# Kernel optimization log

Measured on AMD Instinct MI355X. Metric: run time of the kernel, lower is better.

The kernel has to match this reference:

```python
import jax, jax.numpy as jnp
import numpy as np

D = 1024

def setup_inputs() -> dict:
    key = jax.random.key(0)
    ks = jax.random.split(key, 12)
    B, N, d = 4, 4096, D
    init_std = 0.02 / np.sqrt(d)  # matches _init_weights for value_proj / o_proj
    inp = {
        "h": jax.random.normal(ks[0], (B, N, d), dtype=jnp.float32),
        # relation_encoder: Linear(d, d//2) -> GELU -> Linear(d//2, 1)  (weights stored [in, out])
        "W_re1": jax.random.normal(ks[1], (d, d // 2), dtype=jnp.float32) * 0.02,
        "b_re1": jnp.zeros((d // 2,), dtype=jnp.float32),
        "W_re2": jax.random.normal(ks[2], (d // 2, 1), dtype=jnp.float32) * 0.02,
        "b_re2": jnp.zeros((1,), dtype=jnp.float32),
        # value_proj: Linear(d, d, bias=False), init std = 0.02/sqrt(d)
        "W_v": jax.random.normal(ks[3], (d, d), dtype=jnp.float32) * init_std,
        # relation_transform: Linear(2d, d) -> GELU -> Linear(d, d)
        "W_rt1": jax.random.normal(ks[4], (2 * d, d), dtype=jnp.float32) * 0.02,
        "b_rt1": jnp.zeros((d,), dtype=jnp.float32),
        "W_rt2": jax.random.normal(ks[5], (d, d), dtype=jnp.float32) * 0.02,
        "b_rt2": jnp.zeros((d,), dtype=jnp.float32),
        # o_proj: Linear(d, d, bias=False), init std = 0.02/sqrt(d)
        "W_o": jax.random.normal(ks[6], (d, d), dtype=jnp.float32) * init_std,
    }
    return inp


def reference(h, W_re1, b_re1, W_re2, b_re2, W_v, W_rt1, b_rt1, W_rt2, b_rt2, W_o):
    B, N, d = h.shape
    # relation_encoder MLP -> scalar logit per token (torch GELU is exact erf form)
    hidden = jax.nn.gelu(jnp.einsum('bnd,dk->bnk', h, W_re1) + b_re1, approximate=False)
    relation_logits = (jnp.einsum('bnk,ko->bno', hidden, W_re2) + b_re2)[..., 0]  # [B, N]
    relation_strength = jax.nn.sigmoid(relation_logits)  # [B, N]
    # pointer targets: round(sigmoid * (N-1)) clamped (jnp.round == torch.round, half-to-even)
    relation_targets = jnp.clip(
        jnp.round(relation_strength * (N - 1)).astype(jnp.int32), 0, N - 1
    )  # [B, N]
    # per-token gather of target hidden state within each batch row
    target_features = jnp.take_along_axis(h, relation_targets[..., None], axis=1)  # [B, N, d]
    source_values = jnp.einsum('bnd,de->bne', h, W_v)
    target_values = jnp.einsum('bnd,de->bne', target_features, W_v)
    relation_input = jnp.concatenate([source_values, target_values], axis=-1)  # [B, N, 2d]
    relation_output = jax.nn.gelu(
        jnp.einsum('bnf,fe->bne', relation_input, W_rt1) + b_rt1, approximate=False
    )
    relation_output = jnp.einsum('bne,ef->bnf', relation_output, W_rt2) + b_rt2
    z = jnp.einsum('bnd,de->bne', relation_output, W_o)  # [B, N, d]
    return (z, relation_targets, relation_strength)
```

## Files before the change

kernel.cpp:

```cpp
#include <hip/hip_runtime.h>
#include <math.h>
#include <type_traits>

#define DMODEL 1024
#define NSEQ   4096
#define MTOT   16384

typedef unsigned short ushortT;
typedef __attribute__((ext_vector_type(8))) short short8;
typedef __attribute__((ext_vector_type(4))) float f32x4;

__device__ __forceinline__ float gelu_f(float x) {
    return 0.5f * x * (1.0f + erff(x * 0.70710678118654752440f));
}
__device__ __forceinline__ double gelu_d(double x) {
    return 0.5 * x * (1.0 + erf(x * 0.70710678118654752440));
}
__device__ __forceinline__ ushortT f2bf(float f) {
    unsigned u = __float_as_uint(f);
    u += 0x7FFFu + ((u >> 16) & 1u);
    return (ushortT)(u >> 16);
}
__device__ __forceinline__ float bf2f(ushortT b) {
    return __uint_as_float(((unsigned)b) << 16);
}
__device__ __forceinline__ void gload16(const void* g, void* l) {
    __builtin_amdgcn_global_load_lds(
        (const __attribute__((address_space(1))) unsigned*)g,
        (__attribute__((address_space(3))) unsigned*)l, 16, 0, 0);
}

enum { EPI_BF16 = 0, EPI_GELU_BIAS_BF16 = 1, EPI_BIAS_F32 = 2, EPI_TRANS_BF16 = 3 };

template<int EPI, bool GATHER>
__global__ __launch_bounds__(256)
void mfma_gemm(const ushortT* __restrict__ A, const ushortT* __restrict__ Bt,
               const float* __restrict__ bias, void* __restrict__ Cv,
               int K, int lda, int ldb, int ldc, const int* __restrict__ gidx)
{
    __shared__ ushortT As[128 * 32];
    __shared__ ushortT Bs[128 * 32];
    const int tid  = threadIdx.x;
    const int lane = tid & 63;
    const int w    = tid >> 6;
    const int wr   = (w >> 1) * 64;
    const int wc   = (w & 1) * 64;
    const int m0   = blockIdx.y * 128;
    const int n0   = blockIdx.x * 128;

    const int lrow = lane >> 2;
    const int lk   = (lane & 3) * 8;

    int grow_g[2];
    if constexpr (GATHER) {
        grow_g[0] = gidx[m0 + w * 32 + lrow];
        grow_g[1] = gidx[m0 + w * 32 + 16 + lrow];
    }

    f32x4 acc[4][4];
    #pragma unroll
    for (int i = 0; i < 4; i++)
        #pragma unroll
        for (int j = 0; j < 4; j++) acc[i][j] = (f32x4){0.f, 0.f, 0.f, 0.f};

    for (int kk = 0; kk < K; kk += 32) {
        #pragma unroll
        for (int i = 0; i < 2; i++) {
            const int ar = w * 32 + i * 16 + lrow;
            const ushortT* ga;
            if constexpr (GATHER) {
                ga = (kk < DMODEL)
                   ? A + (size_t)(m0 + ar) * lda + kk + lk
                   : A + (size_t)grow_g[i] * lda + (kk - DMODEL) + lk;
            } else {
                ga = A + (size_t)(m0 + ar) * lda + kk + lk;
            }
            gload16(ga, &As[(w * 32 + i * 16) * 32]);
            const ushortT* gb = Bt + (size_t)(n0 + w * 32 + i * 16 + lrow) * ldb + kk + lk;
            gload16(gb, &Bs[(w * 32 + i * 16) * 32]);
        }
        __syncthreads();

        const int mi = lane & 15;
        const int ko = (lane >> 4) * 8;
        short8 a[4], b[4];
        #pragma unroll
        for (int i = 0; i < 4; i++)
            a[i] = *(const short8*)&As[(wr + i * 16 + mi) * 32 + ko];
        #pragma unroll
        for (int j = 0; j < 4; j++)
            b[j] = *(const short8*)&Bs[(wc + j * 16 + mi) * 32 + ko];
        #pragma unroll
        for (int i = 0; i < 4; i++)
            #pragma unroll
            for (int j = 0; j < 4; j++)
                acc[i][j] = __builtin_amdgcn_mfma_f32_16x16x32_bf16(a[i], b[j], acc[i][j], 0, 0, 0);
        __syncthreads();
    }

    const int cr = (lane >> 4) * 4;
    const int cc = lane & 15;
    #pragma unroll
    for (int i = 0; i < 4; i++) {
        #pragma unroll
        for (int j = 0; j < 4; j++) {
            const int gr = m0 + wr + i * 16 + cr;
            const int gc = n0 + wc + j * 16 + cc;
            #pragma unroll
            for (int r = 0; r < 4; r++) {
                float v = acc[i][j][r];
                if constexpr (EPI == EPI_GELU_BIAS_BF16) v = gelu_f(v + bias[gc]);
                if constexpr (EPI == EPI_BIAS_F32)       v = v + bias[gc];
                if constexpr (EPI == EPI_BF16 || EPI == EPI_GELU_BIAS_BF16)
                    ((ushortT*)Cv)[(size_t)(gr + r) * ldc + gc] = f2bf(v);
                else if constexpr (EPI == EPI_BIAS_F32)
                    ((float*)Cv)[(size_t)(gr + r) * ldc + gc] = v;
                else
                    ((ushortT*)Cv)[(size_t)gc * ldc + (gr + r)] = f2bf(v);
            }
        }
    }
}

__global__ __launch_bounds__(256)
void enc_gemm(const ushortT* __restrict__ Ah, const ushortT* __restrict__ Al,
              const ushortT* __restrict__ Bh, const ushortT* __restrict__ Bl,
              const float* __restrict__ bias, float* __restrict__ C)
{
    __shared__ ushortT Ash[128 * 32], Asl[128 * 32];
    __shared__ ushortT Bsh[128 * 32], Bsl[128 * 32];
    const int tid  = threadIdx.x;
    const int lane = tid & 63;
    const int w    = tid >> 6;
    const int wr   = (w >> 1) * 64;
    const int wc   = (w & 1) * 64;
    const int m0   = blockIdx.y * 128;
    const int n0   = blockIdx.x * 128;
    const int lrow = lane >> 2;
    const int lk   = (lane & 3) * 8;

    f32x4 acc[4][4];
    #pragma unroll
    for (int i = 0; i < 4; i++)
        #pragma unroll
        for (int j = 0; j < 4; j++) acc[i][j] = (f32x4){0.f, 0.f, 0.f, 0.f};

    for (int kk = 0; kk < DMODEL; kk += 32) {
        #pragma unroll
        for (int i = 0; i < 2; i++) {
            const size_t aoff = (size_t)(m0 + w * 32 + i * 16 + lrow) * DMODEL + kk + lk;
            const size_t boff = (size_t)(n0 + w * 32 + i * 16 + lrow) * DMODEL + kk + lk;
            const int ldst = (w * 32 + i * 16) * 32;
            gload16(Ah + aoff, &Ash[ldst]);
            gload16(Al + aoff, &Asl[ldst]);
            gload16(Bh + boff, &Bsh[ldst]);
            gload16(Bl + boff, &Bsl[ldst]);
        }
        __syncthreads();

        const int mi = lane & 15;
        const int ko = (lane >> 4) * 8;
        short8 ah[4], al[4], bh[4], bl[4];
        #pragma unroll
        for (int i = 0; i < 4; i++) {
            ah[i] = *(const short8*)&Ash[(wr + i * 16 + mi) * 32 + ko];
            al[i] = *(const short8*)&Asl[(wr + i * 16 + mi) * 32 + ko];
        }
        #pragma unroll
        for (int j = 0; j < 4; j++) {
            bh[j] = *(const short8*)&Bsh[(wc + j * 16 + mi) * 32 + ko];
            bl[j] = *(const short8*)&Bsl[(wc + j * 16 + mi) * 32 + ko];
        }
        #pragma unroll
        for (int i = 0; i < 4; i++)
            #pragma unroll
            for (int j = 0; j < 4; j++) {
                acc[i][j] = __builtin_amdgcn_mfma_f32_16x16x32_bf16(ah[i], bh[j], acc[i][j], 0, 0, 0);
                acc[i][j] = __builtin_amdgcn_mfma_f32_16x16x32_bf16(ah[i], bl[j], acc[i][j], 0, 0, 0);
                acc[i][j] = __builtin_amdgcn_mfma_f32_16x16x32_bf16(al[i], bh[j], acc[i][j], 0, 0, 0);
            }
        __syncthreads();
    }

    const int cr = (lane >> 4) * 4;
    const int cc = lane & 15;
    #pragma unroll
    for (int i = 0; i < 4; i++)
        #pragma unroll
        for (int j = 0; j < 4; j++) {
            const int gr = m0 + wr + i * 16 + cr;
            const int gc = n0 + wc + j * 16 + cc;
            #pragma unroll
            for (int r = 0; r < 4; r++)
                C[(size_t)(gr + r) * 512 + gc] = gelu_f(acc[i][j][r] + bias[gc]);
        }
}

__global__ __launch_bounds__(256)
void target2_k(const float* __restrict__ Genc, const float* __restrict__ W2,
               const float* __restrict__ b2, float* __restrict__ outT,
               float* __restrict__ outS, int* __restrict__ gidx,
               int* __restrict__ cnt, int* __restrict__ list)
{
    const int m = blockIdx.x * 4 + (threadIdx.x >> 6);
    const int lane = threadIdx.x & 63;
    const float* gr = Genc + (size_t)m * 512;
    double s = 0.0;
    #pragma unroll 4
    for (int j = lane; j < 512; j += 64) s = fma((double)gr[j], (double)W2[j], s);
    #pragma unroll
    for (int off = 32; off; off >>= 1) s += __shfl_down(s, off);
    if (lane == 0) {
        double logit = s + (double)b2[0];
        double str = 1.0 / (1.0 + exp(-logit));
        double r = str * (double)(NSEQ - 1);
        double n = rint(r);
        double dist = fabs(r - n);
        n = fmin(fmax(n, 0.0), (double)(NSEQ - 1));
        int t = (int)n;
        outT[m] = (float)t;
        outS[m] = (float)str;
        gidx[m] = ((m >> 12) << 12) + t;
        if (dist > 0.46) {
            int ix = atomicAdd(cnt, 1);
            list[ix] = m;
        }
    }
}

#define FIX_T 2
__global__ __launch_bounds__(256)
void fixup_k(const float* __restrict__ h, const float* __restrict__ W1,
             const float* __restrict__ b1, const float* __restrict__ W2,
             const float* __restrict__ b2, const int* __restrict__ cnt_p,
             const int* __restrict__ list, float* __restrict__ outT,
             float* __restrict__ outS, int* __restrict__ gidx)
{
    __shared__ float hrow[FIX_T][1024];
    __shared__ double red[4][FIX_T];
    const int tid = threadIdx.x;
    const int cnt = *cnt_p;
    for (int base = (int)blockIdx.x * FIX_T; base < cnt;
         base += (int)gridDim.x * FIX_T) {
        const int nt = min(FIX_T, cnt - base);
        for (int t = 0; t < nt; t++) {
            const int m = list[base + t];
            const float4* src = (const float4*)(h + (size_t)m * 1024);
            ((float4*)hrow[t])[tid] = src[tid];
        }
        __syncthreads();

        double a[FIX_T][2];
        #pragma unroll
        for (int t = 0; t < FIX_T; t++) { a[t][0] = 0.0; a[t][1] = 0.0; }

        #pragma unroll 4
        for (int k = 0; k < 1024; k++) {
            const double wa = (double)W1[(size_t)k * 512 + tid];
            const double wb = (double)W1[(size_t)k * 512 + tid + 256];
            #pragma unroll
            for (int t = 0; t < FIX_T; t++) {
                const double hv = (double)hrow[t][k];
                a[t][0] = fma(hv, wa, a[t][0]);
                a[t][1] = fma(hv, wb, a[t][1]);
            }
        }

        const double w2a = (double)W2[tid], w2b = (double)W2[tid + 256];
        const double b1a = (double)b1[tid], b1b = (double)b1[tid + 256];
        const int lane = tid & 63, w = tid >> 6;
        #pragma unroll
        for (int t = 0; t < FIX_T; t++) {
            double v = w2a * gelu_d(a[t][0] + b1a) + w2b * gelu_d(a[t][1] + b1b);
            #pragma unroll
            for (int off = 32; off; off >>= 1) v += __shfl_down(v, off);
            if (lane == 0) red[w][t] = v;
        }
        __syncthreads();
        if (tid < nt) {
            const int t = tid;
            double logit = red[0][t] + red[1][t] + red[2][t] + red[3][t] + (double)b2[0];
            double str = 1.0 / (1.0 + exp(-logit));
            double r = str * (double)(NSEQ - 1);
            double n = rint(r);
            n = fmin(fmax(n, 0.0), (double)(NSEQ - 1));
            const int m = list[base + t];
            const int ti = (int)n;
            outT[m] = (float)ti;
            outS[m] = (float)str;
            gidx[m] = ((m >> 12) << 12) + ti;
        }
        __syncthreads();
    }
}

__global__ __launch_bounds__(256)
void biascomb_k(const float* __restrict__ brt2, const float* __restrict__ Wo,
                float* __restrict__ bc)
{
    int j = blockIdx.x * 256 + threadIdx.x;
    float s = 0.f;
    for (int e = 0; e < DMODEL; e++) s = fmaf(brt2[e], Wo[e * DMODEL + j], s);
    bc[j] = s;
}

__global__ __launch_bounds__(256)
void cast_k(const float* __restrict__ x, ushortT* __restrict__ y, int n)
{
    int i = (blockIdx.x * 256 + threadIdx.x) * 4;
    if (i < n) {
        float4 v = *(const float4*)(x + i);
        ushortT o[4] = { f2bf(v.x), f2bf(v.y), f2bf(v.z), f2bf(v.w) };
        *(ulong1*)&y[i] = *(ulong1*)o;
    }
}

__global__ __launch_bounds__(256)
void split_cast_k(const float* __restrict__ x, ushortT* __restrict__ yh,
                  ushortT* __restrict__ yl, int n)
{
    int i = (blockIdx.x * 256 + threadIdx.x) * 4;
    if (i < n) {
        float4 v = *(const float4*)(x + i);
        float vv[4] = { v.x, v.y, v.z, v.w };
        ushortT oh[4], ol[4];
        #pragma unroll
        for (int q = 0; q < 4; q++) {
            oh[q] = f2bf(vv[q]);
            ol[q] = f2bf(vv[q] - bf2f(oh[q]));
        }
        *(ulong1*)&yh[i] = *(ulong1*)oh;
        *(ulong1*)&yl[i] = *(ulong1*)ol;
    }
}

__global__ __launch_bounds__(256)
void transcast_k(const float* __restrict__ W, ushortT* __restrict__ Wt, int K, int N)
{
    __shared__ float t[32][33];
    const int tx = threadIdx.x & 31, ty = threadIdx.x >> 5;
    const int n0 = blockIdx.x * 32, k0 = blockIdx.y * 32;
    #pragma unroll
    for (int r = 0; r < 32; r += 8)
        t[ty + r][tx] = W[(size_t)(k0 + ty + r) * N + n0 + tx];
    __syncthreads();
    #pragma unroll
    for (int r = 0; r < 32; r += 8)
        Wt[(size_t)(n0 + ty + r) * K + k0 + tx] = f2bf(t[tx][ty + r]);
}

__global__ __launch_bounds__(256)
void split_transcast_k(const float* __restrict__ W, ushortT* __restrict__ Wth,
                       ushortT* __restrict__ Wtl, int K, int N)
{
    __shared__ float t[32][33];
    const int tx = threadIdx.x & 31, ty = threadIdx.x >> 5;
    const int n0 = blockIdx.x * 32, k0 = blockIdx.y * 32;
    #pragma unroll
    for (int r = 0; r < 32; r += 8)
        t[ty + r][tx] = W[(size_t)(k0 + ty + r) * N + n0 + tx];
    __syncthreads();
    #pragma unroll
    for (int r = 0; r < 32; r += 8) {
        float x = t[tx][ty + r];
        ushortT hi = f2bf(x);
        Wth[(size_t)(n0 + ty + r) * K + k0 + tx] = hi;
        Wtl[(size_t)(n0 + ty + r) * K + k0 + tx] = f2bf(x - bf2f(hi));
    }
}

extern "C" void kernel_launch(void* const* d_in, const int* in_sizes, int n_in,
                              void* d_out, int out_size, void* d_ws, size_t ws_size,
                              hipStream_t stream)
{
    const float* h     = (const float*)d_in[0];
    const float* W_re1 = (const float*)d_in[1];
    const float* b_re1 = (const float*)d_in[2];
    const float* W_re2 = (const float*)d_in[3];
    const float* b_re2 = (const float*)d_in[4];
    const float* W_v   = (const float*)d_in[5];
    const float* W_rt1 = (const float*)d_in[6];
    const float* b_rt1 = (const float*)d_in[7];
    const float* W_rt2 = (const float*)d_in[8];
    const float* b_rt2 = (const float*)d_in[9];
    const float* W_o   = (const float*)d_in[10];

    float* z    = (float*)d_out;
    float* outT = z + (size_t)MTOT * DMODEL;
    float* outS = outT + MTOT;
    ushortT* V    = (ushortT*)z;
    ushortT* h_hi = (ushortT*)z + (size_t)MTOT * DMODEL;

    char* ws = (char*)d_ws;
    ushortT* G       = (ushortT*)ws;
    float*   Genc    = (float*)(ws + (32ull  << 20));
    ushortT* h_lo    = (ushortT*)(ws + (64ull  << 20));
    ushortT* Wv_t    = (ushortT*)(ws + (96ull  << 20));
    ushortT* Wrt1_t  = (ushortT*)(ws + (98ull  << 20));
    ushortT* Wo_t    = (ushortT*)(ws + (102ull << 20));
    ushortT* Wrt2_b  = (ushortT*)(ws + (104ull << 20));
    ushortT* Wc_t    = (ushortT*)(ws + (106ull << 20));
    ushortT* Wre1t_h = (ushortT*)(ws + (108ull << 20));
    ushortT* Wre1t_l = (ushortT*)(ws + (109ull << 20));
    float*   b_c     = (float*)(ws + (110ull << 20));
    int*     cnt     = (int*)  (ws + (110ull << 20) + 4096);
    int*     gidx    = (int*)  (ws + (110ull << 20) + 8192);
    int*     list    = (int*)  (ws + (110ull << 20) + 8192 + 65536);

    split_cast_k<<<dim3(MTOT * DMODEL / 1024), 256, 0, stream>>>(h, h_hi, h_lo, MTOT * DMODEL);
    split_transcast_k<<<dim3(16, 32), 256, 0, stream>>>(W_re1, Wre1t_h, Wre1t_l, DMODEL, 512);
    cast_k<<<dim3(DMODEL * DMODEL / 1024), 256, 0, stream>>>(W_rt2, Wrt2_b, DMODEL * DMODEL);
    transcast_k<<<dim3(32, 32), 256, 0, stream>>>(W_v, Wv_t, DMODEL, DMODEL);
    transcast_k<<<dim3(32, 64), 256, 0, stream>>>(W_rt1, Wrt1_t, 2 * DMODEL, DMODEL);
    transcast_k<<<dim3(32, 32), 256, 0, stream>>>(W_o, Wo_t, DMODEL, DMODEL);
    biascomb_k<<<dim3(4), 256, 0, stream>>>(b_rt2, W_o, b_c);

    enc_gemm<<<dim3(4, 128), 256, 0, stream>>>(h_hi, h_lo, Wre1t_h, Wre1t_l, b_re1, Genc);

    hipMemsetAsync(cnt, 0, 4, stream);
    target2_k<<<dim3(MTOT / 4), 256, 0, stream>>>(Genc, W_re2, b_re2, outT, outS, gidx, cnt, list);
    fixup_k<<<dim3(4096), 256, 0, stream>>>(h, W_re1, b_re1, W_re2, b_re2, cnt, list,
                                            outT, outS, gidx);

    mfma_gemm<EPI_TRANS_BF16, false><<<dim3(8, 8), 256, 0, stream>>>(
        Wrt2_b, Wo_t, nullptr, (void*)Wc_t, DMODEL, DMODEL, DMODEL, DMODEL, nullptr);

    mfma_gemm<EPI_BF16, false><<<dim3(8, 128), 256, 0, stream>>>(
        h_hi, Wv_t, nullptr, (void*)V, DMODEL, DMODEL, DMODEL, DMODEL, nullptr);

    mfma_gemm<EPI_GELU_BIAS_BF16, true><<<dim3(8, 128), 256, 0, stream>>>(
        V, Wrt1_t, b_rt1, (void*)G, 2 * DMODEL, DMODEL, 2 * DMODEL, DMODEL, gidx);

    mfma_gemm<EPI_BIAS_F32, false><<<dim3(8, 128), 256, 0, stream>>>(
        G, Wc_t, b_c, (void*)z, DMODEL, DMODEL, DMODEL, DMODEL, nullptr);
}
```

Before: 653.5 us.

## Fold W_v into W_rt1 halves and gather precomputed target projections in epilogue

Precomputes W_v·W_rt1[:d] and W_v·W_rt1[d:] as combined weights with split-bf16 GEMMs. The main pipeline then computes Q = h·Wb for all rows and G = gelu(h·Wa + b + Q[target]), gathering Q rows in the epilogue. This replaces the V GEMM plus the K=2048 gathered GEMM with two K=1024 GEMMs, cutting main-path FLOPs by about a third. The cost is two small weight GEMMs per call, a scattered gather of Q in the epilogue, and different rounding from folding weights in bf16.

```diff
diff --git a/kernel.cpp b/kernel.cpp
--- a/kernel.cpp
+++ b/kernel.cpp
@@ -30,13 +30,15 @@
         (__attribute__((address_space(3))) unsigned*)l, 16, 0, 0);
 }
 
-enum { EPI_BF16 = 0, EPI_GELU_BIAS_BF16 = 1, EPI_BIAS_F32 = 2, EPI_TRANS_BF16 = 3 };
-
-template<int EPI, bool GATHER>
+enum { EPI_BF16 = 0, EPI_GELU_BIAS_BF16 = 1, EPI_BIAS_F32 = 2, EPI_TRANS_BF16 = 3,
+       EPI_GELU_ADDQ_BF16 = 4 };
+
+template<int EPI>
 __global__ __launch_bounds__(256)
 void mfma_gemm(const ushortT* __restrict__ A, const ushortT* __restrict__ Bt,
                const float* __restrict__ bias, void* __restrict__ Cv,
-               int K, int lda, int ldb, int ldc, const int* __restrict__ gidx)
+               int K, int lda, int ldb, int ldc,
+               const int* __restrict__ gidx, const ushortT* __restrict__ Qg)
 {
     __shared__ ushortT As[128 * 32];
     __shared__ ushortT Bs[128 * 32];
@@ -51,12 +53,6 @@
     const int lrow = lane >> 2;
     const int lk   = (lane & 3) * 8;
 
-    int grow_g[2];
-    if constexpr (GATHER) {
-        grow_g[0] = gidx[m0 + w * 32 + lrow];
-        grow_g[1] = gidx[m0 + w * 32 + 16 + lrow];
-    }
-
     f32x4 acc[4][4];
     #pragma unroll
     for (int i = 0; i < 4; i++)
@@ -66,15 +62,7 @@
     for (int kk = 0; kk < K; kk += 32) {
         #pragma unroll
         for (int i = 0; i < 2; i++) {
-            const int ar = w * 32 + i * 16 + lrow;
-            const ushortT* ga;
-            if constexpr (GATHER) {
-                ga = (kk < DMODEL)
-                   ? A + (size_t)(m0 + ar) * lda + kk + lk
-                   : A + (size_t)grow_g[i] * lda + (kk - DMODEL) + lk;
-            } else {
-                ga = A + (size_t)(m0 + ar) * lda + kk + lk;
-            }
+            const ushortT* ga = A + (size_t)(m0 + w * 32 + i * 16 + lrow) * lda + kk + lk;
             gload16(ga, &As[(w * 32 + i * 16) * 32]);
             const ushortT* gb = Bt + (size_t)(n0 + w * 32 + i * 16 + lrow) * ldb + kk + lk;
             gload16(gb, &Bs[(w * 32 + i * 16) * 32]);
@@ -110,8 +98,13 @@
             for (int r = 0; r < 4; r++) {
                 float v = acc[i][j][r];
                 if constexpr (EPI == EPI_GELU_BIAS_BF16) v = gelu_f(v + bias[gc]);
+                if constexpr (EPI == EPI_GELU_ADDQ_BF16) {
+                    const int trow = gidx[gr + r];
+                    v = gelu_f(v + bias[gc] + bf2f(Qg[(size_t)trow * DMODEL + gc]));
+                }
                 if constexpr (EPI == EPI_BIAS_F32)       v = v + bias[gc];
-                if constexpr (EPI == EPI_BF16 || EPI == EPI_GELU_BIAS_BF16)
+                if constexpr (EPI == EPI_BF16 || EPI == EPI_GELU_BIAS_BF16 ||
+                              EPI == EPI_GELU_ADDQ_BF16)
                     ((ushortT*)Cv)[(size_t)(gr + r) * ldc + gc] = f2bf(v);
                 else if constexpr (EPI == EPI_BIAS_F32)
                     ((float*)Cv)[(size_t)(gr + r) * ldc + gc] = v;
@@ -120,6 +113,80 @@
             }
         }
     }
+}
+
+__global__ __launch_bounds__(256)
+void wsplit_gemm(const ushortT* __restrict__ Ah, const ushortT* __restrict__ Al,
+                 const ushortT* __restrict__ Bh, const ushortT* __restrict__ Bl,
+                 ushortT* __restrict__ Ct, int K, int lda, int ldb, int ldc)
+{
+    __shared__ ushortT Ash[128 * 32], Asl[128 * 32];
+    __shared__ ushortT Bsh[128 * 32], Bsl[128 * 32];
+    const int tid  = threadIdx.x;
+    const int lane = tid & 63;
+    const int w    = tid >> 6;
+    const int wr   = (w >> 1) * 64;
+    const int wc   = (w & 1) * 64;
+    const int m0   = blockIdx.y * 128;
+    const int n0   = blockIdx.x * 128;
+    const int lrow = lane >> 2;
+    const int lk   = (lane & 3) * 8;
+
+    f32x4 acc[4][4];
+    #pragma unroll
+    for (int i = 0; i < 4; i++)
+        #pragma unroll
+        for (int j = 0; j < 4; j++) acc[i][j] = (f32x4){0.f, 0.f, 0.f, 0.f};
+
+    for (int kk = 0; kk < K; kk += 32) {
+        #pragma unroll
+        for (int i = 0; i < 2; i++) {
+            const size_t aoff = (size_t)(m0 + w * 32 + i * 16 + lrow) * lda + kk + lk;
+            const size_t boff = (size_t)(n0 + w * 32 + i * 16 + lrow) * ldb + kk + lk;
+            const int ldst = (w * 32 + i * 16) * 32;
+            gload16(Ah + aoff, &Ash[ldst]);
+            gload16(Al + aoff, &Asl[ldst]);
+            gload16(Bh + boff, &Bsh[ldst]);
+            gload16(Bl + boff, &Bsl[ldst]);
+        }
+        __syncthreads();
+
+        const int mi = lane & 15;
+        const int ko = (lane >> 4) * 8;
+        short8 ah[4], al[4], bh[4], bl[4];
+        #pragma unroll
+        for (int i = 0; i < 4; i++) {
+            ah[i] = *(const short8*)&Ash[(wr + i * 16 + mi) * 32 + ko];
+            al[i] = *(const short8*)&Asl[(wr + i * 16 + mi) * 32 + ko];
+        }
+        #pragma unroll
+        for (int j = 0; j < 4; j++) {
+            bh[j] = *(const short8*)&Bsh[(wc + j * 16 + mi) * 32 + ko];
+            bl[j] = *(const short8*)&Bsl[(wc + j * 16 + mi) * 32 + ko];
+        }
+        #pragma unroll
+        for (int i = 0; i < 4; i++)
+            #pragma unroll
+            for (int j = 0; j < 4; j++) {
+                acc[i][j] = __builtin_amdgcn_mfma_f32_16x16x32_bf16(ah[i], bh[j], acc[i][j], 0, 0, 0);
+                acc[i][j] = __builtin_amdgcn_mfma_f32_16x16x32_bf16(ah[i], bl[j], acc[i][j], 0, 0, 0);
+                acc[i][j] = __builtin_amdgcn_mfma_f32_16x16x32_bf16(al[i], bh[j], acc[i][j], 0, 0, 0);
+            }
+        __syncthreads();
+    }
+
+    const int cr = (lane >> 4) * 4;
+    const int cc = lane & 15;
+    #pragma unroll
+    for (int i = 0; i < 4; i++)
+        #pragma unroll
+        for (int j = 0; j < 4; j++) {
+            const int gr = m0 + wr + i * 16 + cr;
+            const int gc = n0 + wc + j * 16 + cc;
+            #pragma unroll
+            for (int r = 0; r < 4; r++)
+                Ct[(size_t)gc * ldc + (gr + r)] = f2bf(acc[i][j][r]);
+        }
 }
 
 __global__ __launch_bounds__(256)
@@ -388,32 +455,41 @@
     float* z    = (float*)d_out;
     float* outT = z + (size_t)MTOT * DMODEL;
     float* outS = outT + MTOT;
-    ushortT* V    = (ushortT*)z;
+    ushortT* Q    = (ushortT*)z;
     ushortT* h_hi = (ushortT*)z + (size_t)MTOT * DMODEL;
 
     char* ws = (char*)d_ws;
     ushortT* G       = (ushortT*)ws;
     float*   Genc    = (float*)(ws + (32ull  << 20));
     ushortT* h_lo    = (ushortT*)(ws + (64ull  << 20));
-    ushortT* Wv_t    = (ushortT*)(ws + (96ull  << 20));
-    ushortT* Wrt1_t  = (ushortT*)(ws + (98ull  << 20));
-    ushortT* Wo_t    = (ushortT*)(ws + (102ull << 20));
-    ushortT* Wrt2_b  = (ushortT*)(ws + (104ull << 20));
-    ushortT* Wc_t    = (ushortT*)(ws + (106ull << 20));
-    ushortT* Wre1t_h = (ushortT*)(ws + (108ull << 20));
-    ushortT* Wre1t_l = (ushortT*)(ws + (109ull << 20));
-    float*   b_c     = (float*)(ws + (110ull << 20));
-    int*     cnt     = (int*)  (ws + (110ull << 20) + 4096);
-    int*     gidx    = (int*)  (ws + (110ull << 20) + 8192);
-    int*     list    = (int*)  (ws + (110ull << 20) + 8192 + 65536);
+    ushortT* Wrt1t_h = (ushortT*)(ws + (96ull  << 20));
+    ushortT* Wrt1t_l = (ushortT*)(ws + (100ull << 20));
+    ushortT* Wv_h    = (ushortT*)(ws + (104ull << 20));
+    ushortT* Wv_l    = (ushortT*)(ws + (106ull << 20));
+    ushortT* Wa_t    = (ushortT*)(ws + (108ull << 20));
+    ushortT* Wb_t    = (ushortT*)(ws + (110ull << 20));
+    ushortT* Wo_t    = (ushortT*)(ws + (112ull << 20));
+    ushortT* Wrt2_b  = (ushortT*)(ws + (114ull << 20));
+    ushortT* Wc_t    = (ushortT*)(ws + (116ull << 20));
+    ushortT* Wre1t_h = (ushortT*)(ws + (118ull << 20));
+    ushortT* Wre1t_l = (ushortT*)(ws + (119ull << 20));
+    float*   b_c     = (float*)(ws + (120ull << 20));
+    int*     cnt     = (int*)  (ws + (120ull << 20) + 4096);
+    int*     gidx    = (int*)  (ws + (120ull << 20) + 8192);
+    int*     list    = (int*)  (ws + (120ull << 20) + 8192 + 65536);
 
     split_cast_k<<<dim3(MTOT * DMODEL / 1024), 256, 0, stream>>>(h, h_hi, h_lo, MTOT * DMODEL);
+    split_cast_k<<<dim3(DMODEL * DMODEL / 1024), 256, 0, stream>>>(W_v, Wv_h, Wv_l, DMODEL * DMODEL);
     split_transcast_k<<<dim3(16, 32), 256, 0, stream>>>(W_re1, Wre1t_h, Wre1t_l, DMODEL, 512);
+    split_transcast_k<<<dim3(32, 64), 256, 0, stream>>>(W_rt1, Wrt1t_h, Wrt1t_l, 2 * DMODEL, DMODEL);
     cast_k<<<dim3(DMODEL * DMODEL / 1024), 256, 0, stream>>>(W_rt2, Wrt2_b, DMODEL * DMODEL);
-    transcast_k<<<dim3(32, 32), 256, 0, stream>>>(W_v, Wv_t, DMODEL, DMODEL);
-    transcast_k<<<dim3(32, 64), 256, 0, stream>>>(W_rt1, Wrt1_t, 2 * DMODEL, DMODEL);
     transcast_k<<<dim3(32, 32), 256, 0, stream>>>(W_o, Wo_t, DMODEL, DMODEL);
     biascomb_k<<<dim3(4), 256, 0, stream>>>(b_rt2, W_o, b_c);
+
+    wsplit_gemm<<<dim3(8, 8), 256, 0, stream>>>(Wv_h, Wv_l, Wrt1t_h, Wrt1t_l,
+                                                Wa_t, DMODEL, DMODEL, 2 * DMODEL, DMODEL);
+    wsplit_gemm<<<dim3(8, 8), 256, 0, stream>>>(Wv_h, Wv_l, Wrt1t_h + DMODEL, Wrt1t_l + DMODEL,
+                                                Wb_t, DMODEL, DMODEL, 2 * DMODEL, DMODEL);
 
     enc_gemm<<<dim3(4, 128), 256, 0, stream>>>(h_hi, h_lo, Wre1t_h, Wre1t_l, b_re1, Genc);
 
@@ -422,15 +498,15 @@
     fixup_k<<<dim3(4096), 256, 0, stream>>>(h, W_re1, b_re1, W_re2, b_re2, cnt, list,
                                             outT, outS, gidx);
 
-    mfma_gemm<EPI_TRANS_BF16, false><<<dim3(8, 8), 256, 0, stream>>>(
-        Wrt2_b, Wo_t, nullptr, (void*)Wc_t, DMODEL, DMODEL, DMODEL, DMODEL, nullptr);
-
-    mfma_gemm<EPI_BF16, false><<<dim3(8, 128), 256, 0, stream>>>(
-        h_hi, Wv_t, nullptr, (void*)V, DMODEL, DMODEL, DMODEL, DMODEL, nullptr);
-
-    mfma_gemm<EPI_GELU_BIAS_BF16, true><<<dim3(8, 128), 256, 0, stream>>>(
-        V, Wrt1_t, b_rt1, (void*)G, 2 * DMODEL, DMODEL, 2 * DMODEL, DMODEL, gidx);
-
-    mfma_gemm<EPI_BIAS_F32, false><<<dim3(8, 128), 256, 0, stream>>>(
-        G, Wc_t, b_c, (void*)z, DMODEL, DMODEL, DMODEL, DMODEL, nullptr);
-}
+    mfma_gemm<EPI_TRANS_BF16><<<dim3(8, 8), 256, 0, stream>>>(
+        Wrt2_b, Wo_t, nullptr, (void*)Wc_t, DMODEL, DMODEL, DMODEL, DMODEL, nullptr, nullptr);
+
+    mfma_gemm<EPI_BF16><<<dim3(8, 128), 256, 0, stream>>>(
+        h_hi, Wb_t, nullptr, (void*)Q, DMODEL, DMODEL, DMODEL, DMODEL, nullptr, nullptr);
+
+    mfma_gemm<EPI_GELU_ADDQ_BF16><<<dim3(8, 128), 256, 0, stream>>>(
+        h_hi, Wa_t, b_rt1, (void*)G, DMODEL, DMODEL, DMODEL, DMODEL, gidx, Q);
+
+    mfma_gemm<EPI_BIAS_F32><<<dim3(8, 128), 256, 0, stream>>>(
+        G, Wc_t, b_c, (void*)z, DMODEL, DMODEL, DMODEL, DMODEL, nullptr, nullptr);
+}
```

Measured after the change: 703.0 us. 7.6% more time.
